# Kernel tuning notes

Hardware: AMD Instinct MI355X
Metric: run time of the kernel (lower is better)

The kernel has to match this reference:

```python
import jax, jax.numpy as jnp
import numpy as np

NENTITY = 200000
NRELATION = 500
HIDDEN = 256
GAMMA = 12.0
EPS = 2.0
EMB_RANGE = (GAMMA + EPS) / HIDDEN


def setup_inputs() -> dict:
    key = jax.random.key(0)
    ks = jax.random.split(key, 8)
    B, NEG = 256, 1024
    head = jax.random.randint(ks[0], (B, 1), 0, NENTITY)
    tail = jax.random.randint(ks[1], (B, NEG), 0, NENTITY)
    relation = jax.random.randint(ks[2], (B,), 0, NRELATION)
    entity_emb = jax.random.uniform(ks[3], (NENTITY, HIDDEN), jnp.float32, -EMB_RANGE, EMB_RANGE)
    relation_emb = jax.random.uniform(ks[4], (NRELATION, 2 * HIDDEN), jnp.float32, -EMB_RANGE, EMB_RANGE)
    lim = 1.0 / np.sqrt(2 * HIDDEN)
    W_fc = jax.random.uniform(ks[5], (HIDDEN, 2 * HIDDEN), jnp.float32, -lim, lim)
    b_fc = jax.random.uniform(ks[6], (HIDDEN,), jnp.float32, -lim, lim)
    return {"head": head, "tail": tail, "relation": relation,
            "entity_emb": entity_emb, "relation_emb": relation_emb,
            "W_fc": W_fc, "b_fc": b_fc}


def _l2_normalize(x):
    # F.normalize(x, p=2, dim=-1): x / max(||x||_2, 1e-12)
    n = jnp.sqrt(jnp.sum(x * x, axis=-1, keepdims=True))
    return x / jnp.maximum(n, 1e-12)


def reference(head, tail, relation, entity_emb, relation_emb, W_fc, b_fc):
    # gather embeddings
    h = entity_emb[head]                      # [B, 1,   d]
    t = entity_emb[tail]                      # [B, NEG, d]
    r = relation_emb[relation][:, None, :]    # [B, 1, 2d]
    re_head, re_tail = jnp.split(r, 2, axis=-1)   # each [B, 1, d]
    # broadcast relation halves to match head/tail sample counts, then concat
    re_h = jnp.broadcast_to(re_head, h.shape)
    re_t = jnp.broadcast_to(re_tail, t.shape)
    h_cat = jnp.concatenate([h, re_h], axis=-1)   # [B, 1,   2d]
    t_cat = jnp.concatenate([t, re_t], axis=-1)   # [B, NEG, 2d]
    # shared small FC (torch Linear: x @ W^T + b)
    h_fc = jnp.einsum('bnk,dk->bnd', h_cat, W_fc) + b_fc
    t_fc = jnp.einsum('bnk,dk->bnd', t_cat, W_fc) + b_fc
    h_n = _l2_normalize(h_fc)
    t_n = _l2_normalize(t_fc)
    diff = h_n - t_n                              # [B, NEG, d]
    score = GAMMA - jnp.sum(jnp.abs(diff), axis=2)  # [B, NEG]
    return score
```

## Files before the change

### kernel.cpp

```cpp
#include <hip/hip_runtime.h>
#include <math.h>

#define HIDDEN 256
#define NEG 1024
#define NBATCH 256
#define GAMMA_F 12.0f
#define BM 32
#define NTILES 8
#define NBLK 1024

typedef short v8s __attribute__((ext_vector_type(8)));
typedef float v4f __attribute__((ext_vector_type(4)));
typedef unsigned int u32;

#define LDS_BARRIER() asm volatile("s_waitcnt lgkmcnt(0)\n\ts_barrier" ::: "memory")

__device__ __forceinline__ short f2bf(float x) {
    u32 u = __float_as_uint(x);
    u = (u + 0x7fffu + ((u >> 16) & 1u)) >> 16;
    return (short)u;
}

__device__ __forceinline__ u32 rhu(float f) { return __float_as_uint(f) + 0x8000u; }
__device__ __forceinline__ v8s pack8(const float4& x0, const float4& x1) {
    int4 fr;
    fr.x = __builtin_amdgcn_perm(rhu(x0.y), rhu(x0.x), 0x07060302u);
    fr.y = __builtin_amdgcn_perm(rhu(x0.w), rhu(x0.z), 0x07060302u);
    fr.z = __builtin_amdgcn_perm(rhu(x1.y), rhu(x1.x), 0x07060302u);
    fr.w = __builtin_amdgcn_perm(rhu(x1.w), rhu(x1.z), 0x07060302u);
    return __builtin_bit_cast(v8s, fr);
}

__global__ __launch_bounds__(256) void prep_kernel(
    const int* __restrict__ head, const int* __restrict__ relation,
    const float* __restrict__ entity_emb, const float* __restrict__ relation_emb,
    const float* __restrict__ W_fc, const float* __restrict__ b_fc,
    short* __restrict__ W1bf, float* __restrict__ h_n, float* __restrict__ rel_part)
{
    const int b = blockIdx.x;
    const int t = threadIdx.x;

    W1bf[b * HIDDEN + t] = f2bf(W_fc[(size_t)b * 2 * HIDDEN + t]);

    __shared__ float xh[2 * HIDDEN];
    __shared__ float xt[HIDDEN];
    __shared__ float red[256];

    const int hidx = head[b];
    const int r = relation[b];
    xh[t]          = entity_emb[(size_t)hidx * HIDDEN + t];
    xh[HIDDEN + t] = relation_emb[(size_t)r * 2 * HIDDEN + t];
    xt[t]          = relation_emb[(size_t)r * 2 * HIDDEN + HIDDEN + t];
    __syncthreads();

    const float4* wrow = reinterpret_cast<const float4*>(W_fc + (size_t)t * 2 * HIDDEN);
    float hf = b_fc[t];
    float rp = b_fc[t];
    #pragma unroll 4
    for (int kk = 0; kk < HIDDEN / 4; ++kk) {
        float4 w = wrow[kk];
        hf += xh[4*kk+0]*w.x + xh[4*kk+1]*w.y + xh[4*kk+2]*w.z + xh[4*kk+3]*w.w;
    }
    #pragma unroll 4
    for (int kk = 0; kk < HIDDEN / 4; ++kk) {
        float4 w = wrow[HIDDEN/4 + kk];
        hf += xh[HIDDEN+4*kk+0]*w.x + xh[HIDDEN+4*kk+1]*w.y + xh[HIDDEN+4*kk+2]*w.z + xh[HIDDEN+4*kk+3]*w.w;
        rp += xt[4*kk+0]*w.x + xt[4*kk+1]*w.y + xt[4*kk+2]*w.z + xt[4*kk+3]*w.w;
    }
    rel_part[b * HIDDEN + t] = rp;

    red[t] = hf * hf;
    __syncthreads();
    for (int s = 128; s > 0; s >>= 1) {
        if (t < s) red[t] += red[t + s];
        __syncthreads();
    }
    const float norm = sqrtf(red[0]);
    h_n[b * HIDDEN + t] = hf / fmaxf(norm, 1e-12f);
}

__global__ __launch_bounds__(256, 2) void score_kernel(
    const int* __restrict__ tail, const float* __restrict__ entity_emb,
    const short* __restrict__ W1bf, const float* __restrict__ h_n,
    const float* __restrict__ rel_part, float* __restrict__ out)
{
    __shared__ __align__(16) float Asf[2][BM * HIDDEN];
    __shared__ int tails[NTILES * BM];
    __shared__ float ssq_lds[4][BM];
    __shared__ float l1_lds[4][BM];

    const int t = threadIdx.x;
    const int w = t >> 6;
    const int l = t & 63;
    const int c = t & 15;
    const int g = (t >> 4) & 3;
    const int b = blockIdx.x >> 2;

    tails[t] = tail[blockIdx.x * (NTILES * BM) + t];

    float rlv[4], hnv[4];
    #pragma unroll
    for (int ntl = 0; ntl < 4; ++ntl) {
        const int n = 64 * w + ntl * 16 + c;
        rlv[ntl] = rel_part[b * HIDDEN + n];
        hnv[ntl] = h_n[b * HIDDEN + n];
    }

    v8s Bf[4][8];
    #pragma unroll
    for (int ntl = 0; ntl < 4; ++ntl) {
        const short* bsrc = W1bf + (size_t)(64 * w + ntl * 16 + c) * HIDDEN + g * 8;
        #pragma unroll
        for (int kt = 0; kt < 8; ++kt)
            Bf[ntl][kt] = *reinterpret_cast<const v8s*>(bsrc + kt * 32);
    }
    #pragma unroll
    for (int ntl = 0; ntl < 4; ++ntl)
        #pragma unroll
        for (int kt = 0; kt < 8; ++kt)
            asm volatile("" : "+v"(Bf[ntl][kt]));

    __syncthreads();

    v4f st[8];
    auto issue = [&](int j) {
        #pragma unroll
        for (int i = 0; i < 8; ++i) {
            const int r = w * 8 + i;
            const float* src = entity_emb + (size_t)tails[j * BM + r] * HIDDEN + (l << 2);
            st[i] = *reinterpret_cast<const v4f*>(src);
        }
        __builtin_amdgcn_sched_barrier(0);
    };
    auto commit = [&](int buf) {
        #pragma unroll
        for (int i = 0; i < 8; ++i) {
            const int r = w * 8 + i;
            *reinterpret_cast<v4f*>(&Asf[buf][r * HIDDEN + ((l ^ (r & 7)) << 2)]) = st[i];
        }
    };

    issue(0);
    commit(0);
    LDS_BARRIER();

    #pragma unroll 1
    for (int j = 0; j < NTILES; ++j) {
        const int cur = j & 1;

        if (j + 1 < NTILES) issue(j + 1);

        v4f acc[2][4];
        #pragma unroll
        for (int mt = 0; mt < 2; ++mt)
            #pragma unroll
            for (int ntl = 0; ntl < 4; ++ntl)
                acc[mt][ntl] = v4f{0.f, 0.f, 0.f, 0.f};

        const float* a0base = &Asf[cur][c * HIDDEN];
        const float* a1base = &Asf[cur][(16 + c) * HIDDEN];
        const int swz = c & 7;

        #pragma unroll
        for (int kt = 0; kt < 8; ++kt) {
            const int u0 = kt * 8 + g * 2;
            float4 x0 = *reinterpret_cast<const float4*>(a0base + (((u0    ) ^ swz) << 2));
            float4 x1 = *reinterpret_cast<const float4*>(a0base + (((u0 + 1) ^ swz) << 2));
            float4 y0 = *reinterpret_cast<const float4*>(a1base + (((u0    ) ^ swz) << 2));
            float4 y1 = *reinterpret_cast<const float4*>(a1base + (((u0 + 1) ^ swz) << 2));
            v8s a0 = pack8(x0, x1);
            v8s a1 = pack8(y0, y1);
            #pragma unroll
            for (int ntl = 0; ntl < 4; ++ntl) {
                acc[0][ntl] = __builtin_amdgcn_mfma_f32_16x16x32_bf16(a0, Bf[ntl][kt], acc[0][ntl], 0, 0, 0);
                acc[1][ntl] = __builtin_amdgcn_mfma_f32_16x16x32_bf16(a1, Bf[ntl][kt], acc[1][ntl], 0, 0, 0);
            }
        }

        #pragma unroll
        for (int mt = 0; mt < 2; ++mt) {
            float ssq[4] = {0.f, 0.f, 0.f, 0.f};
            #pragma unroll
            for (int ntl = 0; ntl < 4; ++ntl) {
                #pragma unroll
                for (int r = 0; r < 4; ++r) {
                    float tf = acc[mt][ntl][r] + rlv[ntl];
                    acc[mt][ntl][r] = tf;
                    ssq[r] += tf * tf;
                }
            }
            #pragma unroll
            for (int mask = 1; mask < 16; mask <<= 1) {
                #pragma unroll
                for (int r = 0; r < 4; ++r) ssq[r] += __shfl_xor(ssq[r], mask);
            }
            if (c == 0) {
                #pragma unroll
                for (int r = 0; r < 4; ++r) ssq_lds[w][mt * 16 + g * 4 + r] = ssq[r];
            }
        }
        LDS_BARRIER();

        #pragma unroll
        for (int mt = 0; mt < 2; ++mt) {
            float rn[4], s1[4] = {0.f, 0.f, 0.f, 0.f};
            #pragma unroll
            for (int r = 0; r < 4; ++r) {
                const int m = mt * 16 + g * 4 + r;
                float tot = ssq_lds[0][m] + ssq_lds[1][m] + ssq_lds[2][m] + ssq_lds[3][m];
                rn[r] = 1.f / fmaxf(sqrtf(tot), 1e-12f);
            }
            #pragma unroll
            for (int ntl = 0; ntl < 4; ++ntl) {
                #pragma unroll
                for (int r = 0; r < 4; ++r)
                    s1[r] += fabsf(hnv[ntl] - acc[mt][ntl][r] * rn[r]);
            }
            #pragma unroll
            for (int mask = 1; mask < 16; mask <<= 1) {
                #pragma unroll
                for (int r = 0; r < 4; ++r) s1[r] += __shfl_xor(s1[r], mask);
            }
            if (c == 0) {
                #pragma unroll
                for (int r = 0; r < 4; ++r) l1_lds[w][mt * 16 + g * 4 + r] = s1[r];
            }
        }

        if (j + 1 < NTILES) commit(cur ^ 1);
        LDS_BARRIER();

        if (t < BM) {
            out[blockIdx.x * (NTILES * BM) + j * BM + t] = GAMMA_F -
                (l1_lds[0][t] + l1_lds[1][t] + l1_lds[2][t] + l1_lds[3][t]);
        }
    }
}

extern "C" void kernel_launch(void* const* d_in, const int* in_sizes, int n_in,
                              void* d_out, int out_size, void* d_ws, size_t ws_size,
                              hipStream_t stream)
{
    const int*   head         = (const int*)d_in[0];
    const int*   tail         = (const int*)d_in[1];
    const int*   relation     = (const int*)d_in[2];
    const float* entity_emb   = (const float*)d_in[3];
    const float* relation_emb = (const float*)d_in[4];
    const float* W_fc         = (const float*)d_in[5];
    const float* b_fc         = (const float*)d_in[6];
    float* out = (float*)d_out;

    short* W1bf     = (short*)d_ws;
    float* h_n      = (float*)((char*)d_ws + 131072);
    float* rel_part = (float*)((char*)d_ws + 131072 + 262144);

    prep_kernel<<<NBATCH, 256, 0, stream>>>(head, relation, entity_emb, relation_emb,
                                            W_fc, b_fc, W1bf, h_n, rel_part);
    score_kernel<<<NBLK, 256, 0, stream>>>(tail, entity_emb, W1bf,
                                           h_n, rel_part, out);
}
```

Before: 364.5 us.

## Precompute bf16 projection of all entities, then gather projected rows for scoring

Adds a dense projection kernel that multiplies every entity row by the entity half of the FC weight with bf16 MFMA and stores the result as a bf16 table in workspace. A new scoring kernel then gathers 512-byte projected rows per tail, adds the relation part, normalizes and reduces the L1 distance with wave shuffles. There are more tail samples than entities, so this does less matmul work, turns scattered fp32 gathers into a sequential table read plus smaller bf16 gathers, and the ~100MB table may stay in the large last-level cache. In exchange it adds an extra bf16 rounding of the projected values and needs a large workspace; it falls back to the old kernel if the workspace is too small. It also drops the register-pinning asm barriers in the old score kernel.

```diff
diff --git a/kernel.cpp b/kernel.cpp
--- a/kernel.cpp
+++ b/kernel.cpp
@@ -1,6 +1,7 @@
 #include <hip/hip_runtime.h>
 #include <math.h>
 
+#define NENTITY 200000
 #define HIDDEN 256
 #define NEG 1024
 #define NBATCH 256
@@ -8,6 +9,7 @@
 #define BM 32
 #define NTILES 8
 #define NBLK 1024
+#define CHUNK 128
 
 typedef short v8s __attribute__((ext_vector_type(8)));
 typedef float v4f __attribute__((ext_vector_type(4)));
@@ -79,6 +81,137 @@
     h_n[b * HIDDEN + t] = hf / fmaxf(norm, 1e-12f);
 }
 
+__global__ __launch_bounds__(256, 2) void proj_kernel(
+    const float* __restrict__ entity_emb, const short* __restrict__ W1bf,
+    short* __restrict__ P)
+{
+    __shared__ __align__(16) float Asf[BM * HIDDEN];
+
+    const int t = threadIdx.x;
+    const int w = t >> 6;
+    const int l = t & 63;
+    const int c = t & 15;
+    const int g = (t >> 4) & 3;
+    const int R0 = blockIdx.x * BM;
+
+    v8s Bf[4][8];
+    #pragma unroll
+    for (int ntl = 0; ntl < 4; ++ntl) {
+        const short* bsrc = W1bf + (size_t)(64 * w + ntl * 16 + c) * HIDDEN + g * 8;
+        #pragma unroll
+        for (int kt = 0; kt < 8; ++kt)
+            Bf[ntl][kt] = *reinterpret_cast<const v8s*>(bsrc + kt * 32);
+    }
+    #pragma unroll
+    for (int ntl = 0; ntl < 4; ++ntl)
+        #pragma unroll
+        for (int kt = 0; kt < 8; ++kt)
+            asm volatile("" : "+v"(Bf[ntl][kt]));
+
+    v4f st[8];
+    #pragma unroll
+    for (int i = 0; i < 8; ++i) {
+        const int r = w * 8 + i;
+        st[i] = *reinterpret_cast<const v4f*>(
+            entity_emb + (size_t)(R0 + r) * HIDDEN + (l << 2));
+    }
+    __builtin_amdgcn_sched_barrier(0);
+    #pragma unroll
+    for (int i = 0; i < 8; ++i) {
+        const int r = w * 8 + i;
+        *reinterpret_cast<v4f*>(&Asf[r * HIDDEN + ((l ^ (r & 7)) << 2)]) = st[i];
+    }
+    LDS_BARRIER();
+
+    v4f acc[2][4];
+    #pragma unroll
+    for (int mt = 0; mt < 2; ++mt)
+        #pragma unroll
+        for (int ntl = 0; ntl < 4; ++ntl)
+            acc[mt][ntl] = v4f{0.f, 0.f, 0.f, 0.f};
+
+    const float* a0base = &Asf[c * HIDDEN];
+    const float* a1base = &Asf[(16 + c) * HIDDEN];
+    const int swz = c & 7;
+
+    #pragma unroll
+    for (int kt = 0; kt < 8; ++kt) {
+        const int u0 = kt * 8 + g * 2;
+        float4 x0 = *reinterpret_cast<const float4*>(a0base + (((u0    ) ^ swz) << 2));
+        float4 x1 = *reinterpret_cast<const float4*>(a0base + (((u0 + 1) ^ swz) << 2));
+        float4 y0 = *reinterpret_cast<const float4*>(a1base + (((u0    ) ^ swz) << 2));
+        float4 y1 = *reinterpret_cast<const float4*>(a1base + (((u0 + 1) ^ swz) << 2));
+        v8s a0 = pack8(x0, x1);
+        v8s a1 = pack8(y0, y1);
+        #pragma unroll
+        for (int ntl = 0; ntl < 4; ++ntl) {
+            acc[0][ntl] = __builtin_amdgcn_mfma_f32_16x16x32_bf16(a0, Bf[ntl][kt], acc[0][ntl], 0, 0, 0);
+            acc[1][ntl] = __builtin_amdgcn_mfma_f32_16x16x32_bf16(a1, Bf[ntl][kt], acc[1][ntl], 0, 0, 0);
+        }
+    }
+
+    #pragma unroll
+    for (int mt = 0; mt < 2; ++mt)
+        #pragma unroll
+        for (int ntl = 0; ntl < 4; ++ntl)
+            #pragma unroll
+            for (int r = 0; r < 4; ++r) {
+                const int m = mt * 16 + g * 4 + r;
+                const int n = 64 * w + ntl * 16 + c;
+                P[(size_t)(R0 + m) * HIDDEN + n] = f2bf(acc[mt][ntl][r]);
+            }
+}
+
+__global__ __launch_bounds__(256) void score2_kernel(
+    const int* __restrict__ tail, const short* __restrict__ P,
+    const float* __restrict__ h_n, const float* __restrict__ rel_part,
+    float* __restrict__ out)
+{
+    const int t = threadIdx.x;
+    const int w = t >> 6;
+    const int l = t & 63;
+    const int b = blockIdx.x >> 3;
+    const int chunk = blockIdx.x & 7;
+    const int base = b * NEG + chunk * CHUNK;
+
+    __shared__ int tl[CHUNK];
+    if (t < CHUNK) tl[t] = tail[base + t];
+
+    const float4 hh = *reinterpret_cast<const float4*>(h_n + b * HIDDEN + 4 * l);
+    const float4 rp = *reinterpret_cast<const float4*>(rel_part + b * HIDDEN + 4 * l);
+    __syncthreads();
+
+    uint2 st2[8];
+    #pragma unroll
+    for (int i = 0; i < 8; ++i)
+        st2[i] = *(reinterpret_cast<const uint2*>(P + (size_t)tl[w * 32 + i] * HIDDEN) + l);
+
+    #pragma unroll
+    for (int p = 0; p < 32; ++p) {
+        uint2 v = st2[p & 7];
+        if (p + 8 < 32)
+            st2[p & 7] = *(reinterpret_cast<const uint2*>(
+                P + (size_t)tl[w * 32 + p + 8] * HIDDEN) + l);
+
+        float t0 = __uint_as_float(v.x << 16)          + rp.x;
+        float t1 = __uint_as_float(v.x & 0xffff0000u)  + rp.y;
+        float t2 = __uint_as_float(v.y << 16)          + rp.z;
+        float t3 = __uint_as_float(v.y & 0xffff0000u)  + rp.w;
+
+        float ssq = t0 * t0 + t1 * t1 + t2 * t2 + t3 * t3;
+        #pragma unroll
+        for (int mask = 1; mask < 64; mask <<= 1) ssq += __shfl_xor(ssq, mask);
+        const float rn = 1.f / fmaxf(sqrtf(ssq), 1e-12f);
+
+        float l1 = fabsf(hh.x - t0 * rn) + fabsf(hh.y - t1 * rn)
+                 + fabsf(hh.z - t2 * rn) + fabsf(hh.w - t3 * rn);
+        #pragma unroll
+        for (int mask = 1; mask < 64; mask <<= 1) l1 += __shfl_xor(l1, mask);
+
+        if (l == 0) out[base + w * 32 + p] = GAMMA_F - l1;
+    }
+}
+
 __global__ __launch_bounds__(256, 2) void score_kernel(
     const int* __restrict__ tail, const float* __restrict__ entity_emb,
     const short* __restrict__ W1bf, const float* __restrict__ h_n,
@@ -114,11 +247,6 @@
         for (int kt = 0; kt < 8; ++kt)
             Bf[ntl][kt] = *reinterpret_cast<const v8s*>(bsrc + kt * 32);
     }
-    #pragma unroll
-    for (int ntl = 0; ntl < 4; ++ntl)
-        #pragma unroll
-        for (int kt = 0; kt < 8; ++kt)
-            asm volatile("" : "+v"(Bf[ntl][kt]));
 
     __syncthreads();
 
@@ -147,7 +275,6 @@
     #pragma unroll 1
     for (int j = 0; j < NTILES; ++j) {
         const int cur = j & 1;
-
         if (j + 1 < NTILES) issue(j + 1);
 
         v4f acc[2][4];
@@ -256,6 +383,15 @@
 
     prep_kernel<<<NBATCH, 256, 0, stream>>>(head, relation, entity_emb, relation_emb,
                                             W_fc, b_fc, W1bf, h_n, rel_part);
-    score_kernel<<<NBLK, 256, 0, stream>>>(tail, entity_emb, W1bf,
-                                           h_n, rel_part, out);
-}
+
+    const size_t P_OFF   = 1ull << 20;
+    const size_t P_BYTES = (size_t)NENTITY * HIDDEN * sizeof(short);
+    if (ws_size >= P_OFF + P_BYTES) {
+        short* P = (short*)((char*)d_ws + P_OFF);
+        proj_kernel<<<NENTITY / BM, 256, 0, stream>>>(entity_emb, W1bf, P);
+        score2_kernel<<<NBATCH * 8, 256, 0, stream>>>(tail, P, h_n, rel_part, out);
+    } else {
+        score_kernel<<<NBLK, 256, 0, stream>>>(tail, entity_emb, W1bf,
+                                               h_n, rel_part, out);
+    }
+}
```

New measurement: 413.0 us. 1.13x slower.
